# Kernel tuning notes

Hardware: AMD Instinct MI355X
Metric: run time of the kernel (lower is better)

The kernel has to match this reference:

```python
import jax, jax.numpy as jnp
import numpy as np

N_VERT = 20000


def _gather_pad(feat, adj):
    # feat: [B, N, C]; adj: [B, N, K] with 1-based indices, 0 = padding (-> zeros)
    B, N, C = feat.shape
    padded = jnp.concatenate([jnp.zeros((B, 1, C), feat.dtype), feat], axis=1)  # [B, N+1, C]
    return jax.vmap(lambda p, a: p[a])(padded, adj)  # [B, N, K, C]


def setup_inputs() -> dict:
    key = jax.random.key(0)
    ks = jax.random.split(key, 7)
    B, N, K, M, C, O = 4, N_VERT, 16, 9, 64, 64
    x = jax.random.normal(ks[0], (B, N, C), jnp.float32)
    adj = jax.random.randint(ks[1], (B, N, K), 0, N + 1, jnp.int32)  # 0 == no neighbor
    W = jax.random.normal(ks[2], (M, O, C), jnp.float32) * 0.1
    b = jax.random.normal(ks[3], (O,), jnp.float32) * 0.1
    u = jax.random.normal(ks[4], (M, C), jnp.float32) * 0.1
    v = jax.random.normal(ks[5], (M, C), jnp.float32) * 0.1
    c = jax.random.normal(ks[6], (M,), jnp.float32) * 0.1
    return {"x": x, "adj": adj, "W": W, "b": b, "u": u, "v": v, "c": c}


def reference(x, adj, W, b, u, v, c):
    # FEAST graph conv, non-invariant path.
    mask = adj != 0  # [B, N, K]
    # attention logits: u.x_i + v.x_j + c, masked (padding) neighbors -> 0 + c
    ux = jnp.einsum('bnc,mc->bnm', x, u)          # [B, N, M]
    vx = jnp.einsum('bnc,mc->bnm', x, v)          # [B, N, M]
    vxn = _gather_pad(vx, adj)                    # [B, N, K, M]
    logits = jnp.where(mask[..., None], ux[:, :, None, :] + vxn, 0.0) + c
    q = jax.nn.softmax(logits, axis=-1)           # softmax over M kernels
    # gather raw neighbor features (zero for padding), contract q over K first,
    # then apply per-kernel W (linear, so order is equivalent to original wx-gather)
    xn = _gather_pad(x, adj)                      # [B, N, K, C]
    s = jnp.einsum('bnkm,bnkc->bnmc', q, xn)      # [B, N, M, C]
    out = jnp.einsum('bnmc,moc->bno', s, W)       # [B, N, O]
    deg = jnp.sum(mask, axis=-1).astype(x.dtype)  # [B, N]
    inv_deg = jnp.where(deg > 0, 1.0 / jnp.maximum(deg, 1.0), 0.0)
    return out * inv_deg[..., None] + b
```

## Files before the change

kernel.cpp:

```cpp
#include <hip/hip_runtime.h>
#include <cstdint>
#include <cstddef>

#define BB 4
#define NN 20000
#define KK 16
#define MM 9
#define CC 64
#define OO 64
#define BN (BB*NN)
#define MC (MM*CC)
#define UVP 12
#define QNP 272
#define SCP 72
#define SNP (MM*SCP)
#define NKS (MC/32)
#define NCHUNK 625

typedef _Float16 f16x8 __attribute__((ext_vector_type(8)));
typedef _Float16 f16x4 __attribute__((ext_vector_type(4)));
typedef __fp16   fp16v2 __attribute__((ext_vector_type(2)));
typedef float    f32x4 __attribute__((ext_vector_type(4)));
typedef unsigned short u16;
typedef unsigned int   u32;

union Hcv { _Float16 h; u16 u; };
__device__ __forceinline__ u16 f2h(float f) { Hcv t; t.h = (_Float16)f; return t.u; }
__device__ __forceinline__ float h2f(u16 h) { Hcv t; t.u = h; return (float)t.h; }

__global__ __launch_bounds__(256) void pre_kernel(
    const float* __restrict__ x, const float* __restrict__ W,
    const float* __restrict__ u, const float* __restrict__ v,
    const float* __restrict__ c,
    float* __restrict__ uxc, float* __restrict__ vxp,
    u16* __restrict__ xh, u16* __restrict__ wfb2)
{
    const int bid = blockIdx.x;
    if (bid >= 1250) {
        int base = (bid - 1250) * 1024 + threadIdx.x * 4;
        ushort4 wv;
        u16* wp = (u16*)&wv;
        #pragma unroll
        for (int t = 0; t < 4; ++t) {
            int i = base + t;
            int j = i & 7, o = (i >> 3) & 63, l2 = (i >> 9) & 3, ks = i >> 11;
            int kf = ks * 32 + l2 * 8 + j;
            int m = kf >> 6, cc2 = kf & 63;
            wp[t] = f2h(W[m * 4096 + o * 64 + cc2]);
        }
        *(ushort4*)(wfb2 + base) = wv;
        return;
    }
    const int wave = threadIdx.x >> 6, lane = threadIdx.x & 63;
    const int lr = lane & 15, lhi = lane >> 4;
    const int t0n = bid * 64 + wave * 16;

    const float* xr = x + (size_t)(t0n + lr) * 64 + lhi * 8;
    float xf[16];
    *(float4*)(xf + 0)  = *(const float4*)(xr + 0);
    *(float4*)(xf + 4)  = *(const float4*)(xr + 4);
    *(float4*)(xf + 8)  = *(const float4*)(xr + 32);
    *(float4*)(xf + 12) = *(const float4*)(xr + 36);
    union { u16 us[8]; f16x8 v; ushort4 s4[2]; } H0, L0, H1, L1;
    #pragma unroll
    for (int i = 0; i < 8; ++i) {
        u16 h = f2h(xf[i]);      H0.us[i] = h;  L0.us[i] = f2h(xf[i] - h2f(h));
        u16 h2 = f2h(xf[8 + i]); H1.us[i] = h2; L1.us[i] = f2h(xf[8 + i] - h2f(h2));
    }
    *(ushort4*)(xh + (size_t)(t0n + lr) * 64 + lhi * 8)      = H0.s4[0];
    *(ushort4*)(xh + (size_t)(t0n + lr) * 64 + lhi * 8 + 4)  = H0.s4[1];
    *(ushort4*)(xh + (size_t)(t0n + lr) * 64 + 32 + lhi * 8)     = H1.s4[0];
    *(ushort4*)(xh + (size_t)(t0n + lr) * 64 + 32 + lhi * 8 + 4) = H1.s4[1];

    f32x4 acc0 = {0.f,0.f,0.f,0.f}, acc1 = {0.f,0.f,0.f,0.f};
    #pragma unroll
    for (int t = 0; t < 2; ++t) {
        int r = t * 16 + lr;
        const float* gp = (r < 9) ? (u + r * 64) : (v + (r - 9) * 64);
        bool nz = r < 18;
        f32x4 acc = {0.f,0.f,0.f,0.f};
        #pragma unroll
        for (int s = 0; s < 2; ++s) {
            float gf[8];
            *(float4*)(gf + 0) = nz ? *(const float4*)(gp + s * 32 + lhi * 8)
                                    : make_float4(0.f,0.f,0.f,0.f);
            *(float4*)(gf + 4) = nz ? *(const float4*)(gp + s * 32 + lhi * 8 + 4)
                                    : make_float4(0.f,0.f,0.f,0.f);
            union { u16 us[8]; f16x8 v; } GH, GL;
            #pragma unroll
            for (int i = 0; i < 8; ++i) {
                u16 h = f2h(gf[i]); GH.us[i] = h; GL.us[i] = f2h(gf[i] - h2f(h));
            }
            f16x8 as  = s ? H1.v : H0.v;
            f16x8 asl = s ? L1.v : L0.v;
            acc = __builtin_amdgcn_mfma_f32_16x16x32_f16(as,  GH.v, acc, 0, 0, 0);
            acc = __builtin_amdgcn_mfma_f32_16x16x32_f16(as,  GL.v, acc, 0, 0, 0);
            acc = __builtin_amdgcn_mfma_f32_16x16x32_f16(asl, GH.v, acc, 0, 0, 0);
        }
        if (t == 0) acc0 = acc; else acc1 = acc;
    }
    float cv = (lr < 9) ? c[lr] : 0.f;
    #pragma unroll
    for (int reg = 0; reg < 4; ++reg) {
        int node = t0n + lhi * 4 + reg;
        if (lr < 9) uxc[(size_t)node * UVP + lr] = acc0[reg] + cv;
        else        vxp[(size_t)node * UVP + (lr - 9)] = acc0[reg];
        if (lr < 2) vxp[(size_t)node * UVP + 7 + lr] = acc1[reg];
    }
}

__global__ __launch_bounds__(256) void fused_kernel(
    const u16* __restrict__ xh, const int* __restrict__ adj,
    const float* __restrict__ uxc, const float* __restrict__ vxp,
    const u16* __restrict__ wfb2, const float* __restrict__ bias,
    float* __restrict__ out)
{
    __shared__ __align__(16) u16 qlds[32 * QNP];
    __shared__ __align__(16) u16 slds[16 * SNP];
    const int bid = blockIdx.x;
    const int grp = bid & 7;
    const int b = grp >> 1;
    const int chunk = (bid >> 3) * 2 + (grp & 1);
    if (chunk >= NCHUNK) return;
    const int tid = threadIdx.x, wave = tid >> 6, lane = tid & 63;
    const int lr = lane & 15, lhi = lane >> 4;
    const int node0 = b * NN + chunk * 32;
    const int rowbase = b * NN;
    const u16* xhb = xh + ((size_t)rowbase << 6);

    const int g = lhi;
    const int k = lr;
    int jjA[2];
    jjA[0] = adj[(size_t)node0 * KK + tid];
    jjA[1] = adj[(size_t)node0 * KK + 256 + tid];
    #pragma unroll
    for (int t = 0; t < 2; ++t) {
        int jj = jjA[t];
        unsigned long long bal = __ballot(jj != 0);
        int deg = __popcll((bal >> (g * 16)) & 0xffffull);
        float inv = (deg > 0) ? (1.0f / (float)deg) : 0.0f;
        const int node = node0 + t * 16 + wave * 4 + g;
        float q[MM];
        #pragma unroll
        for (int m = 0; m < MM; ++m) q[m] = 0.f;
        if (jj != 0) {
            const float4* ur = (const float4*)(uxc + (size_t)node * UVP);
            const float4* vr = (const float4*)(vxp + ((size_t)rowbase + (jj - 1)) * UVP);
            float4 u0 = ur[0], u1 = ur[1], u2 = ur[2];
            float4 v0 = vr[0], v1 = vr[1], v2 = vr[2];
            float l[MM] = { u0.x+v0.x, u0.y+v0.y, u0.z+v0.z, u0.w+v0.w,
                            u1.x+v1.x, u1.y+v1.y, u1.z+v1.z, u1.w+v1.w,
                            u2.x+v2.x };
            float mx = l[0];
            #pragma unroll
            for (int m = 1; m < MM; ++m) mx = fmaxf(mx, l[m]);
            float sum = 0.f;
            #pragma unroll
            for (int m = 0; m < MM; ++m) { l[m] = __expf(l[m] - mx); sum += l[m]; }
            float sc = inv / sum;
            #pragma unroll
            for (int m = 0; m < MM; ++m) q[m] = l[m] * sc;
        }
        u16* qw = qlds + (t * 16 + wave * 4 + g) * QNP + k;
        #pragma unroll
        for (int m = 0; m < MM; ++m) qw[m * 16] = f2h(q[m]);
    }

    f16x8 idf[2];
    #pragma unroll
    for (int s = 0; s < 2; ++s) {
        union { u16 us[8]; f16x8 v; } t;
        #pragma unroll
        for (int j = 0; j < 8; ++j)
            t.us[j] = (lhi * 8 + j == s * 16 + lr) ? (u16)0x3C00 : (u16)0;
        idf[s] = t.v;
    }

    f16x8 aLo[4], aHi[4];
    f16x4 qf[4];
    #pragma unroll
    for (int g2 = 0; g2 < 4; ++g2) {
        int e = __builtin_amdgcn_ds_bpermute((g2 * 16 + lr) * 4, jjA[0]);
        int erow = ((e > 0) ? e : 1) - 1;
        const u16* rp = xhb + ((size_t)erow << 6) + lhi * 8;
        aLo[g2] = *(const f16x8*)(rp);
        aHi[g2] = *(const f16x8*)(rp + 32);
        qf[g2]  = *(const f16x4*)(qlds + (wave * 4 + g2) * QNP + lr * 16 + lhi * 4);
    }

    #pragma unroll
    for (int g2 = 0; g2 < 4; ++g2) {
        const int rnode = wave * 4 + g2;
        #pragma unroll
        for (int cc = 0; cc < 4; ++cc) {
            f32x4 xt = {0.f,0.f,0.f,0.f};
            xt = __builtin_amdgcn_mfma_f32_16x16x32_f16(
                     (cc < 2) ? aLo[g2] : aHi[g2], idf[cc & 1], xt, 0, 0, 0);
            union { fp16v2 h2[2]; f16x4 h4; } at;
            at.h2[0] = __builtin_amdgcn_cvt_pkrtz(xt[0], xt[1]);
            at.h2[1] = __builtin_amdgcn_cvt_pkrtz(xt[2], xt[3]);
            f32x4 d2 = {0.f,0.f,0.f,0.f};
            d2 = __builtin_amdgcn_mfma_f32_16x16x16f16(at.h4, qf[g2], d2, 0, 0, 0);
            if (lr < 9) {
                u32 lo = __builtin_amdgcn_perm((u32)f2h(d2[1]), (u32)f2h(d2[0]), 0x05040100u);
                u32 hi = __builtin_amdgcn_perm((u32)f2h(d2[3]), (u32)f2h(d2[2]), 0x05040100u);
                uint2* p = (uint2*)(slds + rnode * SNP + lr * SCP + cc * 16 + lhi * 4);
                *p = make_uint2(lo, hi);
            }
        }
    }
    __syncthreads();

    f16x8 bLo[4], bHi[4];
    f16x4 qg[4];
    #pragma unroll
    for (int g2 = 0; g2 < 4; ++g2) {
        int e = __builtin_amdgcn_ds_bpermute((g2 * 16 + lr) * 4, jjA[1]);
        int erow = ((e > 0) ? e : 1) - 1;
        const u16* rp = xhb + ((size_t)erow << 6) + lhi * 8;
        bLo[g2] = *(const f16x8*)(rp);
        bHi[g2] = *(const f16x8*)(rp + 32);
        qg[g2]  = *(const f16x4*)(qlds + (16 + wave * 4 + g2) * QNP + lr * 16 + lhi * 4);
    }

    const int o0 = wave * 16;
    float bv = bias[o0 + lr];
    {
        f32x4 acc = {0.f,0.f,0.f,0.f};
        #pragma unroll
        for (int ks = 0; ks < NKS; ++ks) {
            int kf = ks * 32 + lhi * 8;
            int m = kf >> 6, coff = kf & 63;
            f16x8 afrag = *(const f16x8*)(slds + lr * SNP + m * SCP + coff);
            f16x8 bfrag = *(const f16x8*)(wfb2 + (size_t)(((ks * 4 + lhi) * 64) + o0 + lr) * 8);
            acc = __builtin_amdgcn_mfma_f32_16x16x32_f16(afrag, bfrag, acc, 0, 0, 0);
        }
        #pragma unroll
        for (int reg = 0; reg < 4; ++reg) {
            int rr = node0 + lhi * 4 + reg;
            out[(size_t)rr * OO + o0 + lr] = acc[reg] + bv;
        }
    }
    __syncthreads();

    #pragma unroll
    for (int g2 = 0; g2 < 4; ++g2) {
        const int rnode = wave * 4 + g2;
        #pragma unroll
        for (int cc = 0; cc < 4; ++cc) {
            f32x4 xt = {0.f,0.f,0.f,0.f};
            xt = __builtin_amdgcn_mfma_f32_16x16x32_f16(
                     (cc < 2) ? bLo[g2] : bHi[g2], idf[cc & 1], xt, 0, 0, 0);
            union { fp16v2 h2[2]; f16x4 h4; } at;
            at.h2[0] = __builtin_amdgcn_cvt_pkrtz(xt[0], xt[1]);
            at.h2[1] = __builtin_amdgcn_cvt_pkrtz(xt[2], xt[3]);
            f32x4 d2 = {0.f,0.f,0.f,0.f};
            d2 = __builtin_amdgcn_mfma_f32_16x16x16f16(at.h4, qg[g2], d2, 0, 0, 0);
            if (lr < 9) {
                u32 lo = __builtin_amdgcn_perm((u32)f2h(d2[1]), (u32)f2h(d2[0]), 0x05040100u);
                u32 hi = __builtin_amdgcn_perm((u32)f2h(d2[3]), (u32)f2h(d2[2]), 0x05040100u);
                uint2* p = (uint2*)(slds + rnode * SNP + lr * SCP + cc * 16 + lhi * 4);
                *p = make_uint2(lo, hi);
            }
        }
    }
    __syncthreads();

    {
        f32x4 acc = {0.f,0.f,0.f,0.f};
        #pragma unroll
        for (int ks = 0; ks < NKS; ++ks) {
            int kf = ks * 32 + lhi * 8;
            int m = kf >> 6, coff = kf & 63;
            f16x8 afrag = *(const f16x8*)(slds + lr * SNP + m * SCP + coff);
            f16x8 bfrag = *(const f16x8*)(wfb2 + (size_t)(((ks * 4 + lhi) * 64) + o0 + lr) * 8);
            acc = __builtin_amdgcn_mfma_f32_16x16x32_f16(afrag, bfrag, acc, 0, 0, 0);
        }
        #pragma unroll
        for (int reg = 0; reg < 4; ++reg) {
            int rr = node0 + 16 + lhi * 4 + reg;
            out[(size_t)rr * OO + o0 + lr] = acc[reg] + bv;
        }
    }
}

extern "C" void kernel_launch(void* const* d_in, const int* in_sizes, int n_in,
                              void* d_out, int out_size, void* d_ws, size_t ws_size,
                              hipStream_t stream)
{
    const float* x   = (const float*)d_in[0];
    const int*   adj = (const int*)  d_in[1];
    const float* W   = (const float*)d_in[2];
    const float* b   = (const float*)d_in[3];
    const float* u   = (const float*)d_in[4];
    const float* v   = (const float*)d_in[5];
    const float* c   = (const float*)d_in[6];
    float* out = (float*)d_out;

    float* uxc = (float*)d_ws;
    float* vxp = uxc + (size_t)BN * UVP;
    u16*   xh  = (u16*)(vxp + (size_t)BN * UVP);
    u16*   wfb2= xh + (size_t)BN * CC;

    pre_kernel<<<1286, 256, 0, stream>>>(x, W, u, v, c, uxc, vxp, xh, wfb2);
    fused_kernel<<<2504, 256, 0, stream>>>(xh, adj, uxc, vxp, wfb2, b, out);
}
```

Measured before the change: 133.3 us.

## Halve nodes per block, swizzle S layout in LDS, raise occupancy

Each block now handles 16 nodes instead of 32, which doubles the grid and removes the second half-pass along with its extra syncs. The S staging buffer moves to an XOR-swizzled layout with 16-byte granules to cut LDS bank conflicts on the MFMA A-fragment reads, and LDS use shrinks. The neighbor-row gathers are issued before the softmax so their latency overlaps that computation, and launch bounds now request 6 blocks per SM. In exchange, the per-block setup (identity fragments, bias, W fragment loads) is repeated across twice as many blocks.

```diff
diff --git a/kernel.cpp b/kernel.cpp
--- a/kernel.cpp
+++ b/kernel.cpp
@@ -11,11 +11,10 @@
 #define BN (BB*NN)
 #define MC (MM*CC)
 #define UVP 12
-#define QNP 272
-#define SCP 72
-#define SNP (MM*SCP)
+#define QNP 160
+#define QTAIL 128
 #define NKS (MC/32)
-#define NCHUNK 625
+#define NCHUNK16 1250
 
 typedef _Float16 f16x8 __attribute__((ext_vector_type(8)));
 typedef _Float16 f16x4 __attribute__((ext_vector_type(4)));
@@ -109,37 +108,41 @@
     }
 }
 
-__global__ __launch_bounds__(256) void fused_kernel(
+__global__ __launch_bounds__(256, 6) void fused_kernel(
     const u16* __restrict__ xh, const int* __restrict__ adj,
     const float* __restrict__ uxc, const float* __restrict__ vxp,
     const u16* __restrict__ wfb2, const float* __restrict__ bias,
     float* __restrict__ out)
 {
-    __shared__ __align__(16) u16 qlds[32 * QNP];
-    __shared__ __align__(16) u16 slds[16 * SNP];
+    __shared__ __align__(16) u16 qlds[16 * QNP + QTAIL];
+    __shared__ __align__(16) u16 slds[72 * 16 * 8];
     const int bid = blockIdx.x;
     const int grp = bid & 7;
     const int b = grp >> 1;
     const int chunk = (bid >> 3) * 2 + (grp & 1);
-    if (chunk >= NCHUNK) return;
     const int tid = threadIdx.x, wave = tid >> 6, lane = tid & 63;
     const int lr = lane & 15, lhi = lane >> 4;
-    const int node0 = b * NN + chunk * 32;
+    const int node0 = b * NN + chunk * 16;
     const int rowbase = b * NN;
     const u16* xhb = xh + ((size_t)rowbase << 6);
 
-    const int g = lhi;
-    const int k = lr;
-    int jjA[2];
-    jjA[0] = adj[(size_t)node0 * KK + tid];
-    jjA[1] = adj[(size_t)node0 * KK + 256 + tid];
-    #pragma unroll
-    for (int t = 0; t < 2; ++t) {
-        int jj = jjA[t];
+    int jj = adj[(size_t)node0 * KK + tid];
+
+    f16x8 aLo[4], aHi[4];
+    #pragma unroll
+    for (int g2 = 0; g2 < 4; ++g2) {
+        int e = __builtin_amdgcn_ds_bpermute((g2 * 16 + lr) * 4, jj);
+        int erow = ((e > 0) ? e : 1) - 1;
+        const u16* rp = xhb + ((size_t)erow << 6) + lhi * 8;
+        aLo[g2] = *(const f16x8*)(rp);
+        aHi[g2] = *(const f16x8*)(rp + 32);
+    }
+
+    {
         unsigned long long bal = __ballot(jj != 0);
-        int deg = __popcll((bal >> (g * 16)) & 0xffffull);
+        int deg = __popcll((bal >> (lhi * 16)) & 0xffffull);
         float inv = (deg > 0) ? (1.0f / (float)deg) : 0.0f;
-        const int node = node0 + t * 16 + wave * 4 + g;
+        const int node = node0 + wave * 4 + lhi;
         float q[MM];
         #pragma unroll
         for (int m = 0; m < MM; ++m) q[m] = 0.f;
@@ -161,10 +164,15 @@
             #pragma unroll
             for (int m = 0; m < MM; ++m) q[m] = l[m] * sc;
         }
-        u16* qw = qlds + (t * 16 + wave * 4 + g) * QNP + k;
+        u16* qw = qlds + (wave * 4 + lhi) * QNP + lr;
         #pragma unroll
         for (int m = 0; m < MM; ++m) qw[m * 16] = f2h(q[m]);
     }
+
+    f16x4 qf[4];
+    #pragma unroll
+    for (int g2 = 0; g2 < 4; ++g2)
+        qf[g2] = *(const f16x4*)(qlds + (wave * 4 + g2) * QNP + lr * 16 + lhi * 4);
 
     f16x8 idf[2];
     #pragma unroll
@@ -174,18 +182,6 @@
         for (int j = 0; j < 8; ++j)
             t.us[j] = (lhi * 8 + j == s * 16 + lr) ? (u16)0x3C00 : (u16)0;
         idf[s] = t.v;
-    }
-
-    f16x8 aLo[4], aHi[4];
-    f16x4 qf[4];
-    #pragma unroll
-    for (int g2 = 0; g2 < 4; ++g2) {
-        int e = __builtin_amdgcn_ds_bpermute((g2 * 16 + lr) * 4, jjA[0]);
-        int erow = ((e > 0) ? e : 1) - 1;
-        const u16* rp = xhb + ((size_t)erow << 6) + lhi * 8;
-        aLo[g2] = *(const f16x8*)(rp);
-        aHi[g2] = *(const f16x8*)(rp + 32);
-        qf[g2]  = *(const f16x4*)(qlds + (wave * 4 + g2) * QNP + lr * 16 + lhi * 4);
     }
 
     #pragma unroll
@@ -204,83 +200,29 @@
             if (lr < 9) {
                 u32 lo = __builtin_amdgcn_perm((u32)f2h(d2[1]), (u32)f2h(d2[0]), 0x05040100u);
                 u32 hi = __builtin_amdgcn_perm((u32)f2h(d2[3]), (u32)f2h(d2[2]), 0x05040100u);
-                uint2* p = (uint2*)(slds + rnode * SNP + lr * SCP + cc * 16 + lhi * 4);
-                *p = make_uint2(lo, hi);
+                int q_ = lr * 8 + cc * 2 + (lhi >> 1);
+                int idx16 = (((q_ * 16 + rnode) << 3) ^ ((lr & 7) << 3)) + (lhi & 1) * 4;
+                *(uint2*)(slds + idx16) = make_uint2(lo, hi);
             }
         }
     }
     __syncthreads();
-
-    f16x8 bLo[4], bHi[4];
-    f16x4 qg[4];
-    #pragma unroll
-    for (int g2 = 0; g2 < 4; ++g2) {
-        int e = __builtin_amdgcn_ds_bpermute((g2 * 16 + lr) * 4, jjA[1]);
-        int erow = ((e > 0) ? e : 1) - 1;
-        const u16* rp = xhb + ((size_t)erow << 6) + lhi * 8;
-        bLo[g2] = *(const f16x8*)(rp);
-        bHi[g2] = *(const f16x8*)(rp + 32);
-        qg[g2]  = *(const f16x4*)(qlds + (16 + wave * 4 + g2) * QNP + lr * 16 + lhi * 4);
-    }
 
     const int o0 = wave * 16;
     float bv = bias[o0 + lr];
-    {
-        f32x4 acc = {0.f,0.f,0.f,0.f};
-        #pragma unroll
-        for (int ks = 0; ks < NKS; ++ks) {
-            int kf = ks * 32 + lhi * 8;
-            int m = kf >> 6, coff = kf & 63;
-            f16x8 afrag = *(const f16x8*)(slds + lr * SNP + m * SCP + coff);
-            f16x8 bfrag = *(const f16x8*)(wfb2 + (size_t)(((ks * 4 + lhi) * 64) + o0 + lr) * 8);
-            acc = __builtin_amdgcn_mfma_f32_16x16x32_f16(afrag, bfrag, acc, 0, 0, 0);
-        }
-        #pragma unroll
-        for (int reg = 0; reg < 4; ++reg) {
-            int rr = node0 + lhi * 4 + reg;
-            out[(size_t)rr * OO + o0 + lr] = acc[reg] + bv;
-        }
-    }
-    __syncthreads();
-
-    #pragma unroll
-    for (int g2 = 0; g2 < 4; ++g2) {
-        const int rnode = wave * 4 + g2;
-        #pragma unroll
-        for (int cc = 0; cc < 4; ++cc) {
-            f32x4 xt = {0.f,0.f,0.f,0.f};
-            xt = __builtin_amdgcn_mfma_f32_16x16x32_f16(
-                     (cc < 2) ? bLo[g2] : bHi[g2], idf[cc & 1], xt, 0, 0, 0);
-            union { fp16v2 h2[2]; f16x4 h4; } at;
-            at.h2[0] = __builtin_amdgcn_cvt_pkrtz(xt[0], xt[1]);
-            at.h2[1] = __builtin_amdgcn_cvt_pkrtz(xt[2], xt[3]);
-            f32x4 d2 = {0.f,0.f,0.f,0.f};
-            d2 = __builtin_amdgcn_mfma_f32_16x16x16f16(at.h4, qg[g2], d2, 0, 0, 0);
-            if (lr < 9) {
-                u32 lo = __builtin_amdgcn_perm((u32)f2h(d2[1]), (u32)f2h(d2[0]), 0x05040100u);
-                u32 hi = __builtin_amdgcn_perm((u32)f2h(d2[3]), (u32)f2h(d2[2]), 0x05040100u);
-                uint2* p = (uint2*)(slds + rnode * SNP + lr * SCP + cc * 16 + lhi * 4);
-                *p = make_uint2(lo, hi);
-            }
-        }
-    }
-    __syncthreads();
-
-    {
-        f32x4 acc = {0.f,0.f,0.f,0.f};
-        #pragma unroll
-        for (int ks = 0; ks < NKS; ++ks) {
-            int kf = ks * 32 + lhi * 8;
-            int m = kf >> 6, coff = kf & 63;
-            f16x8 afrag = *(const f16x8*)(slds + lr * SNP + m * SCP + coff);
-            f16x8 bfrag = *(const f16x8*)(wfb2 + (size_t)(((ks * 4 + lhi) * 64) + o0 + lr) * 8);
-            acc = __builtin_amdgcn_mfma_f32_16x16x32_f16(afrag, bfrag, acc, 0, 0, 0);
-        }
-        #pragma unroll
-        for (int reg = 0; reg < 4; ++reg) {
-            int rr = node0 + 16 + lhi * 4 + reg;
-            out[(size_t)rr * OO + o0 + lr] = acc[reg] + bv;
-        }
+    f32x4 acc = {0.f,0.f,0.f,0.f};
+    #pragma unroll
+    for (int ks = 0; ks < NKS; ++ks) {
+        int q_ = ks * 4 + lhi;
+        int idx16 = ((q_ * 16 + lr) << 3) ^ (((q_ >> 3) & 7) << 3);
+        f16x8 afrag = *(const f16x8*)(slds + idx16);
+        f16x8 bfrag = *(const f16x8*)(wfb2 + (size_t)(((ks * 4 + lhi) * 64) + o0 + lr) * 8);
+        acc = __builtin_amdgcn_mfma_f32_16x16x32_f16(afrag, bfrag, acc, 0, 0, 0);
+    }
+    #pragma unroll
+    for (int reg = 0; reg < 4; ++reg) {
+        int rr = node0 + lhi * 4 + reg;
+        out[(size_t)rr * OO + o0 + lr] = acc[reg] + bv;
     }
 }
 
@@ -303,5 +245,5 @@
     u16*   wfb2= xh + (size_t)BN * CC;
 
     pre_kernel<<<1286, 256, 0, stream>>>(x, W, u, v, c, uxc, vxp, xh, wfb2);
-    fused_kernel<<<2504, 256, 0, stream>>>(xh, adj, uxc, vxp, wfb2, b, out);
+    fused_kernel<<<5000, 256, 0, stream>>>(xh, adj, uxc, vxp, wfb2, b, out);
 }
```

Result: no change. 131.8 us (-1.1%).
